# Optimization experiments

Hardware: AMD Instinct MI355X
Metric: run time of the kernel (lower is better)

The kernel has to match this reference:

```python
import jax, jax.numpy as jnp
import numpy as np

N_NODES = 20000
N_EDGES = 320000
N_RELS = 200
DESC_LEN = 16
DIM_G = 64
DIM_WORD = 300
DIM_HIDDEN = 256
H_DIR = DIM_HIDDEN // 2  # per-direction GRU hidden
N_CLASS = 2000
V_WORD = 30000
V_DESC = 30000
B, T = 4, 32


def setup_inputs() -> dict:
    key = jax.random.key(0)
    ks = jax.random.split(key, 24)
    inp = {}
    # index tensors (pad token is 0; generate tokens in [1, V) so all positions valid)
    inp['questions'] = jax.random.randint(ks[0], (B, T), 1, V_WORD)
    inp['node_descs'] = jax.random.randint(ks[1], (N_NODES, DESC_LEN), 1, V_DESC)
    inp['edge_src'] = jax.random.randint(ks[2], (N_EDGES,), 0, N_NODES)
    inp['edge_dst'] = jax.random.randint(ks[3], (N_EDGES,), 0, N_NODES)
    inp['edge_type'] = jax.random.randint(ks[4], (N_EDGES,), 0, N_RELS)
    # embeddings (normal with std 1/sqrt(dim) as in original init)
    inp['emb_word'] = jax.random.normal(ks[5], (V_WORD, DIM_WORD)) / np.sqrt(DIM_WORD)
    inp['emb_desc'] = jax.random.normal(ks[6], (V_DESC, DIM_G)) / np.sqrt(DIM_G)
    # BiGRU params (gates order r,z,n; concatenated along last dim)
    s = 0.1
    inp['Wx_f'] = jax.random.normal(ks[7], (DIM_WORD, 3 * H_DIR)) * s
    inp['Wh_f'] = jax.random.normal(ks[8], (H_DIR, 3 * H_DIR)) * s
    inp['bx_f'] = jnp.zeros((3 * H_DIR,))
    inp['bh_f'] = jnp.zeros((3 * H_DIR,))
    inp['Wx_b'] = jax.random.normal(ks[9], (DIM_WORD, 3 * H_DIR)) * s
    inp['Wh_b'] = jax.random.normal(ks[10], (H_DIR, 3 * H_DIR)) * s
    inp['bx_b'] = jnp.zeros((3 * H_DIR,))
    inp['bh_b'] = jnp.zeros((3 * H_DIR,))
    # lin_h_to_g (kaiming-ish scale)
    inp['W_hg'] = jax.random.normal(ks[11], (DIM_HIDDEN, DIM_G)) * np.sqrt(2.0 / DIM_HIDDEN)
    inp['b_hg'] = jnp.zeros((DIM_G,))
    # RGCN basis decomposition
    inp['bases'] = jax.random.normal(ks[12], (1, DIM_G, DIM_G)) * np.sqrt(1.0 / DIM_G)
    inp['w_comp'] = jax.random.normal(ks[13], (N_RELS, 1))
    inp['rgcn_bias'] = jnp.zeros((DIM_G,))
    # classifier
    inp['W1'] = jax.random.normal(ks[14], (DIM_G + DIM_HIDDEN, 1024)) * np.sqrt(2.0 / (DIM_G + DIM_HIDDEN))
    inp['b1'] = jnp.zeros((1024,))
    inp['W2'] = jax.random.normal(ks[15], (1024, N_CLASS)) * np.sqrt(2.0 / 1024)
    inp['b2'] = jnp.zeros((N_CLASS,))
    return inp


def _gru_last_hidden(x, mask, Wx, Wh, bx, bh):
    """Run a GRU over time; hidden only updates where mask is True.
    x: [B,T,D], mask: [B,T]. Returns final hidden [B,H]."""
    bsz = x.shape[0]
    h0 = jnp.zeros((bsz, Wh.shape[0]), x.dtype)
    gx_all = x @ Wx + bx  # [B,T,3H] precompute input gates

    def step(h, inputs):
        gx, mt = inputs  # [B,3H], [B]
        gh = h @ Wh + bh
        xr, xz, xn = jnp.split(gx, 3, axis=-1)
        hr, hz, hn = jnp.split(gh, 3, axis=-1)
        r = jax.nn.sigmoid(xr + hr)
        z = jax.nn.sigmoid(xz + hz)
        n = jnp.tanh(xn + r * hn)
        h_new = (1.0 - z) * n + z * h
        h = jnp.where(mt[:, None], h_new, h)
        return h, None

    hT, _ = jax.lax.scan(step, h0, (gx_all.transpose(1, 0, 2), mask.T))
    return hT


def _rel_graph_conv(h, edge_src, edge_dst, edge_type, bases, w_comp, bias):
    """Basis-decomposed RGCN layer (DGL RelGraphConv, norm=None, no self-loop).
    h: [B,N,G]. W_r = sum_k w_comp[r,k] * bases[k]."""
    n = h.shape[1]
    # project through each basis first: [B,N,K,O]
    hb = jnp.einsum('bng,kgo->bnko', h, bases)
    # per-edge message: gather src, combine with relation coefficients -> [B,E,O]
    msg = jnp.einsum('beko,ek->beo', hb[:, edge_src], w_comp[edge_type])
    # scatter-add to destination nodes
    agg = jax.vmap(lambda m: jax.ops.segment_sum(m, edge_dst, num_segments=n))(msg)
    return jax.nn.relu(agg + bias)


def reference(questions, node_descs, edge_src, edge_dst, edge_type,
              emb_word, emb_desc,
              Wx_f, Wh_f, bx_f, bh_f, Wx_b, Wh_b, bx_b, bh_b,
              W_hg, b_hg, bases, w_comp, rgcn_bias,
              W1, b1, W2, b2):
    # ---- question encoding (BiGRU over non-pad tokens; pad id = 0) ----
    mask = questions != 0  # [B,T]
    x = emb_word[questions]  # [B,T,Dw] (dropout is identity at eval)
    hf = _gru_last_hidden(x, mask, Wx_f, Wh_f, bx_f, bh_f)
    hb = _gru_last_hidden(x[:, ::-1], mask[:, ::-1], Wx_b, Wh_b, bx_b, bh_b)
    q_emb = jnp.concatenate([hf, hb], axis=-1)  # [B, dim_hidden]

    # ---- attention-weighted node features from descriptions ----
    desc_emb = emb_desc[node_descs]          # [N,L,G]
    q_g = q_emb @ W_hg + b_hg                # [B,G]
    attn1 = jax.nn.softmax(jnp.einsum('nlg,bg->bnl', desc_emb, q_g), axis=-1)
    node_feat = jnp.einsum('bnl,nlg->bng', attn1, desc_emb)  # [B,N,G]

    # ---- one RGCN hidden layer over the KB graph ----
    node_feat = _rel_graph_conv(node_feat, edge_src, edge_dst, edge_type,
                                bases, w_comp, rgcn_bias)

    # ---- attention pooling over nodes ----
    attn2 = jax.nn.softmax(jnp.einsum('bng,bg->bn', node_feat, q_g), axis=1)
    node_agg = jnp.einsum('bn,bng->bg', attn2, node_feat)    # [B,G]

    # ---- classifier ----
    feat = jnp.concatenate([node_agg, q_emb], axis=-1)       # [B, G+H]
    logits = jax.nn.relu(feat @ W1 + b1) @ W2 + b2           # [B, n_class]
    return logits
```

## Files before the change

kernel.cpp:

```cpp
#include <hip/hip_runtime.h>
#include <hip/hip_bf16.h>
#include <math.h>

typedef __hip_bfloat16 bf16;

#define NNODES 20000
#define NEDGES 320000
#define DLEN   16
#define G      64
#define DW     300
#define DH     256
#define HD     128
#define G3     384
#define NCLS   2000
#define NB     4
#define TT     32
#define VDESC  30000
#define NPART  5000
#define A2MID  64

#define NBLK_CVT   384
#define NBLK_GX2   1536
#define NBLK_DESCB (VDESC / 16)
#define NBLK_HIST  ((NEDGES + 255) / 256)
#define NBLK_W2T   (32 * 16)
#define NBLK_SCAT  ((NEDGES + 255) / 256)
#define NBLK_A1    (NNODES / 16)
#define NBLK_DQ    ((VDESC + 63) / 64)

__device__ __forceinline__ float ld(const float* p, size_t i) { return p[i]; }
__device__ __forceinline__ float ld(const bf16* p, size_t i) { return __bfloat162float(p[i]); }
__device__ __forceinline__ void st(float* p, size_t i, float v) { p[i] = v; }
__device__ __forceinline__ void st(bf16* p, size_t i, float v) { p[i] = __float2bfloat16(v); }
__device__ __forceinline__ float relu(float x) { return (x < 0.f) ? 0.f : x; }

#define OFF_FLAG  ((size_t)0)
#define OFF_GX    (OFF_FLAG + 4)
#define OFF_WHF   (OFF_GX   + 2*NB*TT*G3)
#define OFF_QEMB  (OFF_WHF  + 2*HD*G3)
#define OFF_QG    (OFF_QEMB + NB*DH)
#define OFF_HB    (OFF_QG   + NB*G)
#define OFF_DESCB (OFF_HB   + (size_t)NB*NNODES*G/2)
#define OFF_DQ    (OFF_DESCB + (size_t)VDESC*G/2)
#define OFF_PART  (OFF_DQ   + (size_t)VDESC*NB)
#define OFF_PART2 (OFF_PART + (size_t)NPART*NB*66)
#define OFF_DEG   (OFF_PART2+ (size_t)A2MID*NB*66)
#define OFF_OFFS  (OFF_DEG  + NNODES)
#define OFF_RANK  (OFF_OFFS + NNODES + 8)
#define OFF_EPACK (OFF_RANK + NEDGES)
#define OFF_HID   (OFF_EPACK + 2*(size_t)NEDGES)
#define OFF_W2T   (OFF_HID  + 4096)

__global__ void k_init(const unsigned* probe, int* flag, int* deg) {
    int i = blockIdx.x * 256 + threadIdx.x;
    if (i < NNODES) deg[i] = 0;
    if (blockIdx.x == 0 && threadIdx.x < 64) {
        int cnt = 0;
        for (int k = threadIdx.x; k < 4096; k += 64) {
            unsigned lo = probe[k] & 0xFFFFu;
            unsigned e = (lo >> 7) & 0xFFu;
            cnt += (e >= 0x66u && e <= 0x7Eu) ? 1 : 0;
        }
#pragma unroll
        for (int off = 1; off < 64; off <<= 1) cnt += __shfl_xor(cnt, off, 64);
        if (threadIdx.x == 0) *flag = (2 * cnt > 4096) ? 1 : 0;
    }
}

template <typename T>
__device__ void cvt_body(int id, const void* Whf_, const void* Whb_, float* whf) {
    if (id >= 2 * HD * G3) return;
    int d = id / (HD * G3), r = id % (HD * G3);
    const T* W = (const T*)(d ? Whb_ : Whf_);
    whf[id] = ld(W, (size_t)r);
}

template <typename T>
__device__ void gx2_body(int bx2, const int* questions, const void* emb_word_,
                         const void* Wxf_, const void* bxf_,
                         const void* Wxb_, const void* bxb_, float* gx,
                         float* xs, float* psum) {
    int tid = threadIdx.x;
    int jt = bx2 % 6;
    int rid = bx2 / 6;
    int step = rid & 31;
    int b = (rid >> 5) & 3;
    int d = rid >> 7;
    int t = d ? (TT - 1 - step) : step;
    int tok = questions[b * TT + t];
    const T* row = (const T*)emb_word_ + (size_t)tok * DW;
    for (int k = tid; k < DW; k += 256) xs[k] = ld(row, (size_t)k);
    __syncthreads();
    int lane = tid & 63, phase = tid >> 6;
    int j = jt * 64 + lane;
    const T* Wx = (const T*)(d ? Wxb_ : Wxf_);
    float acc = 0.f;
    int k0 = phase * 75;
#pragma unroll 15
    for (int kk = 0; kk < 75; kk++) {
        int k = k0 + kk;
        acc += xs[k] * ld(Wx, (size_t)k * G3 + j);
    }
    psum[tid] = acc;
    __syncthreads();
    if (phase == 0) {
        const T* bx = (const T*)(d ? bxb_ : bxf_);
        float tot = ld(bx, (size_t)j)
                  + psum[lane] + psum[64 + lane] + psum[128 + lane] + psum[192 + lane];
        gx[(size_t)rid * G3 + j] = tot;
    }
}

template <typename T>
__device__ void descb_body(int bx3, const void* emb_desc_, const void* bases_,
                           bf16* descB, float* bsm, float* rsm) {
    int tid = threadIdx.x;
    const T* bases = (const T*)bases_;
    const T* desc = (const T*)emb_desc_;
    for (int i = tid; i < G * G; i += 256) bsm[(i >> 6) * 68 + (i & 63)] = ld(bases, (size_t)i);
    int r0 = bx3 * 16;
    for (int i = tid; i < 16 * G; i += 256) {
        int r = i >> 6, k = i & 63;
        rsm[r * 68 + k] = ld(desc, (size_t)(r0 + r) * G + k);
    }
    __syncthreads();
    int g = tid & 63, slot = tid >> 6;
#pragma unroll
    for (int it = 0; it < 4; it++) {
        int r = slot * 4 + it;
        float acc = 0.f;
#pragma unroll 8
        for (int k = 0; k < G; k++) acc = fmaf(rsm[r * 68 + k], bsm[k * 68 + g], acc);
        descB[(size_t)(r0 + r) * G + g] = __float2bfloat16(acc);
    }
}

template <typename T>
__device__ void w2t_body(int bx5, const void* W2_, float* w2t, float* tile ) {
    int tid = threadIdx.x;
    int ct = bx5 >> 4, ut = bx5 & 15;
    int c0 = ct * 64, u0 = ut * 64;
    int lane = tid & 63, slot = tid >> 6;
    const T* W2 = (const T*)W2_;
    int c = c0 + lane;
    bool okc = (c < NCLS);
#pragma unroll
    for (int i = 0; i < 16; i++) {
        int u = slot * 16 + i;
        tile[u * 65 + lane] = okc ? ld(W2, (size_t)(u0 + u) * NCLS + c) : 0.f;
    }
    __syncthreads();
#pragma unroll
    for (int i = 0; i < 16; i++) {
        int cl = slot * 16 + i;
        if (c0 + cl < NCLS)
            w2t[(size_t)(c0 + cl) * 1024 + u0 + lane] = tile[lane * 65 + cl];
    }
}

__global__ void k_prep(const int* flag, const void* Whf, const void* Whb, float* whf,
                       const int* questions, const void* emb_word,
                       const void* Wxf, const void* bxf,
                       const void* Wxb, const void* bxb, float* gx,
                       const void* emb_desc, const void* bases, bf16* descB,
                       const int* edge_dst, int* deg, int* rank,
                       const void* W2, float* w2t) {
    __shared__ __align__(16) float smem[64 * 68 + 16 * 68];
    int bx = blockIdx.x;
    int tid = threadIdx.x;
    if (bx < NBLK_CVT) {
        int id = bx * 256 + tid;
        if (*flag) cvt_body<bf16>(id, Whf, Whb, whf);
        else       cvt_body<float>(id, Whf, Whb, whf);
    } else if (bx < NBLK_CVT + NBLK_GX2) {
        int bx2 = bx - NBLK_CVT;
        float* xs = smem;
        float* psum = smem + 320;
        if (*flag) gx2_body<bf16>(bx2, questions, emb_word, Wxf, bxf, Wxb, bxb, gx, xs, psum);
        else       gx2_body<float>(bx2, questions, emb_word, Wxf, bxf, Wxb, bxb, gx, xs, psum);
    } else if (bx < NBLK_CVT + NBLK_GX2 + NBLK_DESCB) {
        int bx3 = bx - NBLK_CVT - NBLK_GX2;
        float* bsm = smem;
        float* rsm = smem + 64 * 68;
        if (*flag) descb_body<bf16>(bx3, emb_desc, bases, descB, bsm, rsm);
        else       descb_body<float>(bx3, emb_desc, bases, descB, bsm, rsm);
    } else if (bx < NBLK_CVT + NBLK_GX2 + NBLK_DESCB + NBLK_HIST) {
        int e = (bx - NBLK_CVT - NBLK_GX2 - NBLK_DESCB) * 256 + tid;
        if (e < NEDGES) rank[e] = atomicAdd(&deg[edge_dst[e]], 1);
    } else {
        int bx5 = bx - NBLK_CVT - NBLK_GX2 - NBLK_DESCB - NBLK_HIST;
        if (*flag) w2t_body<bf16>(bx5, W2, w2t, smem);
        else       w2t_body<float>(bx5, W2, w2t, smem);
    }
}

template <typename T>
__device__ void gru_body(const int* questions, const float* gx, const float* whf,
                         const void* bhf_, const void* bhb_, float* qemb,
                         float* hsm, float* ghs) {
    int tid = threadIdx.x;
    int d = blockIdx.x >> 2, b = blockIdx.x & 3;
    int half = tid / G3, j = tid - half * G3;
    const float* wh = whf + (size_t)d * HD * G3 + (size_t)half * 64 * G3 + j;
    float w[64];
#pragma unroll
    for (int m = 0; m < 64; m++) w[m] = wh[(size_t)m * G3];
    const T* bh = (const T*)(d ? bhb_ : bhf_);
    float bhj = (half == 0) ? ld(bh, (size_t)j) : 0.f;
    if (tid < HD) hsm[tid] = 0.f;
    const float* gxb = gx + ((size_t)(d * NB + b)) * TT * G3;
    __syncthreads();
    const float4* h4 = (const float4*)(hsm + half * 64);
    for (int step = 0; step < TT; step++) {
        float acc = bhj;
#pragma unroll
        for (int m4 = 0; m4 < 16; m4++) {
            float4 hp = h4[m4];
            acc = fmaf(hp.x, w[4 * m4 + 0], acc);
            acc = fmaf(hp.y, w[4 * m4 + 1], acc);
            acc = fmaf(hp.z, w[4 * m4 + 2], acc);
            acc = fmaf(hp.w, w[4 * m4 + 3], acc);
        }
        ghs[half * G3 + j] = acc;
        __syncthreads();
        if (tid < HD) {
            const float* gxp = gxb + step * G3;
            int t = d ? (TT - 1 - step) : step;
            bool msk = questions[b * TT + t] != 0;
            float gr = ghs[tid] + ghs[G3 + tid];
            float gz = ghs[HD + tid] + ghs[G3 + HD + tid];
            float gn = ghs[2 * HD + tid] + ghs[G3 + 2 * HD + tid];
            float r = 1.f / (1.f + expf(-(gxp[tid] + gr)));
            float z = 1.f / (1.f + expf(-(gxp[HD + tid] + gz)));
            float n = tanhf(gxp[2 * HD + tid] + r * gn);
            float hn = (1.f - z) * n + z * hsm[tid];
            if (msk) hsm[tid] = hn;
        }
        __syncthreads();
    }
    if (tid < HD) qemb[b * DH + d * HD + tid] = hsm[tid];
}

__device__ void scan_body(const int* deg, int* offs, int* wtot) {
    int t = threadIdx.x;
    int lane = t & 63, wave = t >> 6;
    int c[27];
    int base = t * 27;
    int run = 0;
#pragma unroll
    for (int i = 0; i < 27; i++) {
        int v = (base + i < NNODES) ? deg[base + i] : 0;
        c[i] = run;
        run += v;
    }
    int myrun = run, inc = run;
#pragma unroll
    for (int off = 1; off < 64; off <<= 1) {
        int u = __shfl_up(inc, off, 64);
        if (lane >= off) inc += u;
    }
    if (lane == 63) wtot[wave] = inc;
    __syncthreads();
    if (t == 0) {
        int s = 0;
#pragma unroll
        for (int i = 0; i < 12; i++) { int v = wtot[i]; wtot[i] = s; s += v; }
        offs[NNODES] = s;
    }
    __syncthreads();
    int ebase = wtot[wave] + inc - myrun;
#pragma unroll
    for (int i = 0; i < 27; i++) {
        if (base + i < NNODES) offs[base + i] = ebase + c[i];
    }
}

__global__ __launch_bounds__(2 * G3) void k_gru(const int* flag, const int* questions,
                                                const float* gx, const float* whf,
                                                const void* bhf, const void* bhb, float* qemb,
                                                const int* deg, int* offs) {
    __shared__ __align__(16) float hsm[HD];
    __shared__ float ghs[2 * G3];
    __shared__ int wtot[12];
    if (blockIdx.x < 8) {
        if (*flag) gru_body<bf16>(questions, gx, whf, bhf, bhb, qemb, hsm, ghs);
        else       gru_body<float>(questions, gx, whf, bhf, bhb, qemb, hsm, ghs);
    } else {
        scan_body(deg, offs, wtot);
    }
}

template <typename T>
__device__ void qg_compute(const float* qemb, const void* W_hg_, const void* b_hg_,
                           float* out ) {
    int tid = threadIdx.x;
    int b = tid >> 6, g = tid & 63;
    const T* W = (const T*)W_hg_;
    float acc = ld((const T*)b_hg_, (size_t)g);
#pragma unroll 4
    for (int i = 0; i < DH; i++) acc += qemb[b * DH + i] * ld(W, (size_t)i * G + g);
    out[b * G + g] = acc;
}

template <typename T>
__device__ void dq_body(int chunk, const void* emb_desc_, const float* qgs, float* dq) {
    int tid = threadIdx.x;
    int ii = tid >> 2, b = tid & 3;
    int idx = chunk * 64 + ii;
    if (idx >= VDESC) return;
    const T* row = (const T*)emb_desc_ + (size_t)idx * G;
    const float* q = qgs + b * G;
    float acc = 0.f;
#pragma unroll 8
    for (int k = 0; k < G; k++) acc = fmaf(ld(row, (size_t)k), q[k], acc);
    dq[(size_t)idx * NB + b] = acc;
}

__global__ __launch_bounds__(256) void k_qg_dq(const int* flag, const float* qemb,
                                               const void* W_hg, const void* b_hg, float* qg,
                                               const void* emb_desc, float* dq) {
    __shared__ float qgs[NB * G];
    if (blockIdx.x == 0) {
        if (*flag) qg_compute<bf16>(qemb, W_hg, b_hg, qg);
        else       qg_compute<float>(qemb, W_hg, b_hg, qg);
        return;
    }
    if (*flag) qg_compute<bf16>(qemb, W_hg, b_hg, qgs);
    else       qg_compute<float>(qemb, W_hg, b_hg, qgs);
    __syncthreads();
    int chunk = blockIdx.x - 1;
    if (*flag) dq_body<bf16>(chunk, emb_desc, qgs, dq);
    else       dq_body<float>(chunk, emb_desc, qgs, dq);
}

template <typename T>
__device__ void scatter_body(int e, const int* src, const int* dst, const int* typ,
                             const void* w_comp_, const int* offs, const int* rank,
                             int2* epack) {
    if (e < NEDGES) {
        int pos = offs[dst[e]] + rank[e];
        int2 v;
        v.x = src[e];
        v.y = __float_as_int(ld((const T*)w_comp_, (size_t)typ[e]));
        epack[pos] = v;
    }
}

__device__ void attn1_body(int nb4, const int* node_descs, const float* dq,
                           const bf16* descB, bf16* hb16, float* attn_s, int* idxs) {
    int tid = threadIdx.x;
    int w = tid >> 6, lane = tid & 63;
    int n = nb4 * 4 + w;
    int b = lane >> 4, l = lane & 15;
    const int* nd = node_descs + n * DLEN;
    int idx = nd[l];
    float logit = dq[(size_t)idx * NB + b];
    float mx = logit;
#pragma unroll
    for (int off = 1; off < 16; off <<= 1) mx = fmaxf(mx, __shfl_xor(mx, off, 64));
    float e = expf(logit - mx);
    float s = e;
#pragma unroll
    for (int off = 1; off < 16; off <<= 1) s += __shfl_xor(s, off, 64);
    attn_s[w * 64 + lane] = e / s;
    if (lane < 16) idxs[w * 16 + lane] = idx;
    __syncthreads();
    float o0 = 0.f, o1 = 0.f, o2 = 0.f, o3 = 0.f;
#pragma unroll
    for (int ll = 0; ll < DLEN; ll++) {
        int row = idxs[w * 16 + ll];
        float v = __bfloat162float(descB[(size_t)row * G + lane]);
        o0 = fmaf(attn_s[w * 64 + ll], v, o0);
        o1 = fmaf(attn_s[w * 64 + 16 + ll], v, o1);
        o2 = fmaf(attn_s[w * 64 + 32 + ll], v, o2);
        o3 = fmaf(attn_s[w * 64 + 48 + ll], v, o3);
    }
    size_t baseo = (size_t)n * (NB * G) + lane;
    hb16[baseo + 0 * G] = __float2bfloat16(o0);
    hb16[baseo + 1 * G] = __float2bfloat16(o1);
    hb16[baseo + 2 * G] = __float2bfloat16(o2);
    hb16[baseo + 3 * G] = __float2bfloat16(o3);
}

__global__ __launch_bounds__(256) void k_sc_attn1(const int* flag,
                                                  const int* src, const int* dst, const int* typ,
                                                  const void* w_comp, const int* offs,
                                                  const int* rank, int2* epack,
                                                  const int* node_descs, const float* dq,
                                                  const bf16* descB, bf16* hb16) {
    __shared__ float attn_s[4 * 64];
    __shared__ int idxs[4 * DLEN];
    int bx = blockIdx.x;
    if (bx < NBLK_SCAT) {
        int e = bx * 256 + threadIdx.x;
        if (*flag) scatter_body<bf16>(e, src, dst, typ, w_comp, offs, rank, epack);
        else       scatter_body<float>(e, src, dst, typ, w_comp, offs, rank, epack);
    } else {
        int base = (bx - NBLK_SCAT) * 4;
        for (int it = 0; it < 4; it++) {
            if (it) __syncthreads();
            attn1_body(base + it, node_descs, dq, descB, hb16, attn_s, idxs);
        }
    }
}

__device__ __forceinline__ void a2_update(float& M, float& L, float& A, float p, float v) {
    if (p > M) {
        float s = expf(M - p);
        A *= s; L *= s; M = p;
    }
    float e = expf(p - M);
    L += e;
    A = fmaf(e, v, A);
}

template <typename T>
__device__ void agg_body(const bf16* hb16, const int* offs, const int2* epack,
                         const void* bias_, const float* qg, float* part) {
    int tid = threadIdx.x;
    int b = tid >> 6, g = tid & 63;
    int boff = b * G + g;
    float bias = ld((const T*)bias_, (size_t)g);
    float q = qg[b * G + g];
    float M = -3.4e38f, L = 0.f, A = 0.f;
#pragma unroll 1
    for (int it = 0; it < 4; it++) {
        int dn = blockIdx.x * 4 + it;
        int s0 = offs[dn], s1 = offs[dn + 1];
        float acc = 0.f;
        int p = s0;
        for (; p + 15 < s1; p += 16) {
            int2 ev[16]; float x[16];
#pragma unroll
            for (int k = 0; k < 16; k++) ev[k] = epack[p + k];
#pragma unroll
            for (int k = 0; k < 16; k++)
                x[k] = __bfloat162float(hb16[(size_t)ev[k].x * (NB * G) + boff]);
#pragma unroll
            for (int k = 0; k < 16; k++) acc += __int_as_float(ev[k].y) * x[k];
        }
        for (; p + 7 < s1; p += 8) {
            int2 ev[8]; float x[8];
#pragma unroll
            for (int k = 0; k < 8; k++) ev[k] = epack[p + k];
#pragma unroll
            for (int k = 0; k < 8; k++)
                x[k] = __bfloat162float(hb16[(size_t)ev[k].x * (NB * G) + boff]);
#pragma unroll
            for (int k = 0; k < 8; k++) acc += __int_as_float(ev[k].y) * x[k];
        }
        for (; p + 3 < s1; p += 4) {
            int2 ev[4]; float x[4];
#pragma unroll
            for (int k = 0; k < 4; k++) ev[k] = epack[p + k];
#pragma unroll
            for (int k = 0; k < 4; k++)
                x[k] = __bfloat162float(hb16[(size_t)ev[k].x * (NB * G) + boff]);
#pragma unroll
            for (int k = 0; k < 4; k++) acc += __int_as_float(ev[k].y) * x[k];
        }
        for (; p < s1; p++) {
            int2 ev = epack[p];
            acc += __int_as_float(ev.y) * __bfloat162float(hb16[(size_t)ev.x * (NB * G) + boff]);
        }
        float v = relu(acc + bias);
        float pl = v * q;
#pragma unroll
        for (int off = 32; off >= 1; off >>= 1) pl += __shfl_xor(pl, off, 64);
        a2_update(M, L, A, pl, v);
    }
    float* pp = part + ((size_t)blockIdx.x * NB + b) * 66;
    if (g == 0) { pp[0] = M; pp[1] = L; }
    pp[2 + g] = A;
}
__global__ __launch_bounds__(256) void k_agg(const int* flag, const bf16* hb16, const int* offs,
                                             const int2* epack, const void* bias,
                                             const float* qg, float* part) {
    if (*flag) agg_body<bf16>(hb16, offs, epack, bias, qg, part);
    else       agg_body<float>(hb16, offs, epack, bias, qg, part);
}

__global__ __launch_bounds__(256) void k_attn2m(const float* part, float* part2) {
    int tid = threadIdx.x;
    int b = tid >> 6, lane = tid & 63;
    int grp = blockIdx.x;
    const int per = (NPART + A2MID - 1) / A2MID;
    int start = grp * per;
    int end = (start + per < NPART) ? (start + per) : NPART;
    float M = -3.4e38f, L = 0.f, A = 0.f;
    for (int i = start; i < end; i++) {
        const float* pp = part + ((size_t)i * NB + b) * 66;
        float m = pp[0], l = pp[1], a = pp[2 + lane];
        float mn = fmaxf(M, m);
        float e1 = expf(M - mn), e2 = expf(m - mn);
        A = A * e1 + a * e2;
        L = L * e1 + l * e2;
        M = mn;
    }
    float* pq = part2 + ((size_t)grp * NB + b) * 66;
    if (lane == 0) { pq[0] = M; pq[1] = L; }
    pq[2 + lane] = A;
}

template <typename T>
__device__ void fc1_body(const float* part2, const float* qemb,
                         const void* W1_, const void* b1_, float* hid,
                         float* feat, float* psum) {
    int tid = threadIdx.x;
    int b = blockIdx.x >> 4, tile = blockIdx.x & 15;
    if (tid < 64) {
        float M = -3.4e38f, L = 0.f, A = 0.f;
        for (int p = 0; p < A2MID; p++) {
            const float* pp = part2 + ((size_t)p * NB + b) * 66;
            float m = pp[0], l = pp[1], a = pp[2 + tid];
            float mn = fmaxf(M, m);
            float e1 = expf(M - mn), e2 = expf(m - mn);
            A = A * e1 + a * e2;
            L = L * e1 + l * e2;
            M = mn;
        }
        feat[tid] = A / L;
        feat[tid + 256] = qemb[b * DH + tid + 192];
    } else {
        feat[tid] = qemb[b * DH + tid - G];
    }
    __syncthreads();
    int lane = tid & 63, phase = tid >> 6;
    int u = tile * 64 + lane;
    const T* W1 = (const T*)W1_;
    float acc = 0.f;
#pragma unroll 8
    for (int kk = 0; kk < 80; kk++) {
        int k = phase * 80 + kk;
        acc += feat[k] * ld(W1, (size_t)k * 1024 + u);
    }
    psum[tid] = acc;
    __syncthreads();
    if (phase == 0) {
        float tot = psum[lane] + psum[64 + lane] + psum[128 + lane] + psum[192 + lane]
                  + ld((const T*)b1_, (size_t)u);
        hid[b * 1024 + u] = relu(tot);
    }
}
__global__ __launch_bounds__(256) void k_fc1(const int* flag, const float* part2,
                                             const float* qemb, const void* W1, const void* b1,
                                             float* hid) {
    __shared__ float feat[320];
    __shared__ float psum[256];
    if (*flag) fc1_body<bf16>(part2, qemb, W1, b1, hid, feat, psum);
    else       fc1_body<float>(part2, qemb, W1, b1, hid, feat, psum);
}

template <typename T>
__device__ void fc2_body(const float* hid, const float* w2t, const void* b2_, void* out_,
                         float* hs) {
    int tid = threadIdx.x;
    for (int i = tid; i < 4096; i += 256) hs[i] = hid[i];
    __syncthreads();
    int lane = tid & 63, w = tid >> 6;
#pragma unroll
    for (int itc = 0; itc < 2; itc++) {
        int c = blockIdx.x * 8 + w * 2 + itc;
        const float* wrow = w2t + (size_t)c * 1024;
        float a0 = 0.f, a1 = 0.f, a2 = 0.f, a3 = 0.f;
#pragma unroll
        for (int i = 0; i < 16; i++) {
            int u = i * 64 + lane;
            float wv = wrow[u];
            a0 = fmaf(wv, hs[u], a0);
            a1 = fmaf(wv, hs[1024 + u], a1);
            a2 = fmaf(wv, hs[2048 + u], a2);
            a3 = fmaf(wv, hs[3072 + u], a3);
        }
#pragma unroll
        for (int off = 32; off >= 1; off >>= 1) {
            a0 += __shfl_xor(a0, off, 64);
            a1 += __shfl_xor(a1, off, 64);
            a2 += __shfl_xor(a2, off, 64);
            a3 += __shfl_xor(a3, off, 64);
        }
        if (lane < 4) {
            float av = (lane == 0) ? a0 : (lane == 1) ? a1 : (lane == 2) ? a2 : a3;
            st((T*)out_, (size_t)lane * NCLS + c, av + ld((const T*)b2_, (size_t)c));
        }
    }
}
__global__ __launch_bounds__(256) void k_fc2(const int* flag, const float* hid,
                                             const float* w2t, const void* b2v, void* out) {
    __shared__ float hs[4096];
    if (*flag) fc2_body<bf16>(hid, w2t, b2v, out, hs);
    else       fc2_body<float>(hid, w2t, b2v, out, hs);
}

extern "C" void kernel_launch(void* const* d_in, const int* in_sizes, int n_in,
                              void* d_out, int out_size, void* d_ws, size_t ws_size,
                              hipStream_t stream) {
    const int* questions  = (const int*)d_in[0];
    const int* node_descs = (const int*)d_in[1];
    const int* edge_src   = (const int*)d_in[2];
    const int* edge_dst   = (const int*)d_in[3];
    const int* edge_type  = (const int*)d_in[4];
    const void* emb_word  = d_in[5];
    const void* emb_desc  = d_in[6];
    const void* Wx_f = d_in[7];
    const void* Wh_f = d_in[8];
    const void* bx_f = d_in[9];
    const void* bh_f = d_in[10];
    const void* Wx_b = d_in[11];
    const void* Wh_b = d_in[12];
    const void* bx_b = d_in[13];
    const void* bh_b = d_in[14];
    const void* W_hg = d_in[15];
    const void* b_hg = d_in[16];
    const void* bases = d_in[17];
    const void* w_comp = d_in[18];
    const void* rgcn_bias = d_in[19];
    const void* W1 = d_in[20];
    const void* b1 = d_in[21];
    const void* W2 = d_in[22];
    const void* b2 = d_in[23];

    float* ws = (float*)d_ws;
    int*      flag  = (int*)(ws + OFF_FLAG);
    float*    gx    = ws + OFF_GX;
    float*    whf   = ws + OFF_WHF;
    float*    qemb  = ws + OFF_QEMB;
    float*    qg    = ws + OFF_QG;
    bf16*     hb16  = (bf16*)(ws + OFF_HB);
    bf16*     descB = (bf16*)(ws + OFF_DESCB);
    float*    dq    = ws + OFF_DQ;
    float*    part  = ws + OFF_PART;
    float*    part2 = ws + OFF_PART2;
    int*      deg   = (int*)(ws + OFF_DEG);
    int*      offs  = (int*)(ws + OFF_OFFS);
    int*      rank  = (int*)(ws + OFF_RANK);
    int2*     epack = (int2*)(ws + OFF_EPACK);
    float*    hid   = ws + OFF_HID;
    float*    w2t   = ws + OFF_W2T;

    hipLaunchKernelGGL(k_init, dim3(80), dim3(256), 0, stream,
                       (const unsigned*)emb_word, flag, deg);
    hipLaunchKernelGGL(k_prep,
                       dim3(NBLK_CVT + NBLK_GX2 + NBLK_DESCB + NBLK_HIST + NBLK_W2T),
                       dim3(256), 0, stream,
                       flag, Wh_f, Wh_b, whf,
                       questions, emb_word, Wx_f, bx_f, Wx_b, bx_b, gx,
                       emb_desc, bases, descB,
                       edge_dst, deg, rank, W2, w2t);
    hipLaunchKernelGGL(k_gru, dim3(9), dim3(2 * G3), 0, stream,
                       flag, questions, gx, whf, bh_f, bh_b, qemb, deg, offs);
    hipLaunchKernelGGL(k_qg_dq, dim3(1 + NBLK_DQ), dim3(256), 0, stream,
                       flag, qemb, W_hg, b_hg, qg, emb_desc, dq);
    hipLaunchKernelGGL(k_sc_attn1, dim3(NBLK_SCAT + NBLK_A1), dim3(256), 0, stream,
                       flag, edge_src, edge_dst, edge_type, w_comp, offs, rank, epack,
                       node_descs, dq, descB, hb16);
    hipLaunchKernelGGL(k_agg, dim3(NPART), dim3(256), 0, stream,
                       flag, hb16, offs, epack, rgcn_bias, qg, part);
    hipLaunchKernelGGL(k_attn2m, dim3(A2MID), dim3(256), 0, stream, part, part2);
    hipLaunchKernelGGL(k_fc1, dim3(NB * 16), dim3(256), 0, stream,
                       flag, part2, qemb, W1, b1, hid);
    hipLaunchKernelGGL(k_fc2, dim3(NCLS / 8), dim3(256), 0, stream,
                       flag, hid, w2t, b2, d_out);
}
```

Before: 326.6 us.

## Restructure RGCN aggregation to wave-per-node with LDS-staged edges and vector loads

The aggregation kernel now assigns one wavefront per destination node, with each lane handling 4 features of one batch via 8-byte vector loads of bf16 rows. The block's edge list is staged into shared memory before the gather. The per-block online softmax merge is done through shared memory after all four waves finish. Separately, the attention-1 blocks now process one node group per block instead of four, which quadruples that grid. The aim is fewer, wider gather loads and more parallelism, at the cost of extra syncs and shared-memory traffic.

```diff
diff --git a/kernel.cpp b/kernel.cpp
--- a/kernel.cpp
+++ b/kernel.cpp
@@ -18,6 +18,7 @@
 #define VDESC  30000
 #define NPART  5000
 #define A2MID  64
+#define MAXE   1024
 
 #define NBLK_CVT   384
 #define NBLK_GX2   1536
@@ -25,7 +26,7 @@
 #define NBLK_HIST  ((NEDGES + 255) / 256)
 #define NBLK_W2T   (32 * 16)
 #define NBLK_SCAT  ((NEDGES + 255) / 256)
-#define NBLK_A1    (NNODES / 16)
+#define NBLK_A1    (NNODES / 4)
 #define NBLK_DQ    ((VDESC + 63) / 64)
 
 __device__ __forceinline__ float ld(const float* p, size_t i) { return p[i]; }
@@ -33,6 +34,8 @@
 __device__ __forceinline__ void st(float* p, size_t i, float v) { p[i] = v; }
 __device__ __forceinline__ void st(bf16* p, size_t i, float v) { p[i] = __float2bfloat16(v); }
 __device__ __forceinline__ float relu(float x) { return (x < 0.f) ? 0.f : x; }
+__device__ __forceinline__ float bflo(unsigned u) { return __uint_as_float(u << 16); }
+__device__ __forceinline__ float bfhi(unsigned u) { return __uint_as_float(u & 0xffff0000u); }
 
 #define OFF_FLAG  ((size_t)0)
 #define OFF_GX    (OFF_FLAG + 4)
@@ -396,88 +399,95 @@
         if (*flag) scatter_body<bf16>(e, src, dst, typ, w_comp, offs, rank, epack);
         else       scatter_body<float>(e, src, dst, typ, w_comp, offs, rank, epack);
     } else {
-        int base = (bx - NBLK_SCAT) * 4;
-        for (int it = 0; it < 4; it++) {
-            if (it) __syncthreads();
-            attn1_body(base + it, node_descs, dq, descB, hb16, attn_s, idxs);
-        }
-    }
-}
-
-__device__ __forceinline__ void a2_update(float& M, float& L, float& A, float p, float v) {
-    if (p > M) {
-        float s = expf(M - p);
-        A *= s; L *= s; M = p;
-    }
-    float e = expf(p - M);
-    L += e;
-    A = fmaf(e, v, A);
+        attn1_body(bx - NBLK_SCAT, node_descs, dq, descB, hb16, attn_s, idxs);
+    }
 }
 
 template <typename T>
 __device__ void agg_body(const bf16* hb16, const int* offs, const int2* epack,
-                         const void* bias_, const float* qg, float* part) {
-    int tid = threadIdx.x;
-    int b = tid >> 6, g = tid & 63;
-    int boff = b * G + g;
-    float bias = ld((const T*)bias_, (size_t)g);
-    float q = qg[b * G + g];
+                         const void* bias_, const float* qg, float* part,
+                         int2* eL, float* pm ) {
+    int tid = threadIdx.x;
+    int w = tid >> 6, lane = tid & 63;
+    int b = lane >> 4, g0 = (lane & 15) << 2;
+    int nb = blockIdx.x * 4;
+    int e0 = offs[nb], e1 = offs[nb + 4];
+    int ne = e1 - e0;
+    int dn = nb + w;
+    int s0 = offs[dn] - e0, s1 = offs[dn + 1] - e0;
+    const char* hbase = (const char*)hb16 + (size_t)(b * G + g0) * 2;
+    float a0 = 0.f, a1 = 0.f, a2 = 0.f, a3 = 0.f;
+    for (int base = 0; base < ne; base += MAXE) {
+        int cnt = min(MAXE, ne - base);
+        __syncthreads();
+        for (int i = tid; i < cnt; i += 256) eL[i] = epack[(size_t)e0 + base + i];
+        __syncthreads();
+        int lo = max(s0 - base, 0), hi = min(s1 - base, cnt);
+        int p = lo;
+        for (; p + 7 < hi; p += 8) {
+            uint2 x[8]; float wv[8];
+#pragma unroll
+            for (int k = 0; k < 8; k++) {
+                int2 ev = eL[p + k];
+                wv[k] = __int_as_float(ev.y);
+                x[k] = *(const uint2*)(hbase + ((size_t)ev.x << 9));
+            }
+#pragma unroll
+            for (int k = 0; k < 8; k++) {
+                a0 = fmaf(wv[k], bflo(x[k].x), a0);
+                a1 = fmaf(wv[k], bfhi(x[k].x), a1);
+                a2 = fmaf(wv[k], bflo(x[k].y), a2);
+                a3 = fmaf(wv[k], bfhi(x[k].y), a3);
+            }
+        }
+        for (; p < hi; p++) {
+            int2 ev = eL[p];
+            float wvv = __int_as_float(ev.y);
+            uint2 x = *(const uint2*)(hbase + ((size_t)ev.x << 9));
+            a0 = fmaf(wvv, bflo(x.x), a0);
+            a1 = fmaf(wvv, bfhi(x.x), a1);
+            a2 = fmaf(wvv, bflo(x.y), a2);
+            a3 = fmaf(wvv, bfhi(x.y), a3);
+        }
+    }
+    float v0 = relu(a0 + ld((const T*)bias_, (size_t)(g0 + 0)));
+    float v1 = relu(a1 + ld((const T*)bias_, (size_t)(g0 + 1)));
+    float v2 = relu(a2 + ld((const T*)bias_, (size_t)(g0 + 2)));
+    float v3 = relu(a3 + ld((const T*)bias_, (size_t)(g0 + 3)));
+    const float* qb = qg + b * G + g0;
+    float pl = v0 * qb[0] + v1 * qb[1] + v2 * qb[2] + v3 * qb[3];
+#pragma unroll
+    for (int off = 1; off < 16; off <<= 1) pl += __shfl_xor(pl, off, 64);
+    float* pw = pm + (w * 4 + b) * 66;
+    pw[2 + g0 + 0] = v0;
+    pw[2 + g0 + 1] = v1;
+    pw[2 + g0 + 2] = v2;
+    pw[2 + g0 + 3] = v3;
+    if ((lane & 15) == 0) { pw[0] = pl; pw[1] = 1.f; }
+    __syncthreads();
+    int mb = tid >> 6, g = tid & 63;
     float M = -3.4e38f, L = 0.f, A = 0.f;
-#pragma unroll 1
-    for (int it = 0; it < 4; it++) {
-        int dn = blockIdx.x * 4 + it;
-        int s0 = offs[dn], s1 = offs[dn + 1];
-        float acc = 0.f;
-        int p = s0;
-        for (; p + 15 < s1; p += 16) {
-            int2 ev[16]; float x[16];
-#pragma unroll
-            for (int k = 0; k < 16; k++) ev[k] = epack[p + k];
-#pragma unroll
-            for (int k = 0; k < 16; k++)
-                x[k] = __bfloat162float(hb16[(size_t)ev[k].x * (NB * G) + boff]);
-#pragma unroll
-            for (int k = 0; k < 16; k++) acc += __int_as_float(ev[k].y) * x[k];
-        }
-        for (; p + 7 < s1; p += 8) {
-            int2 ev[8]; float x[8];
-#pragma unroll
-            for (int k = 0; k < 8; k++) ev[k] = epack[p + k];
-#pragma unroll
-            for (int k = 0; k < 8; k++)
-                x[k] = __bfloat162float(hb16[(size_t)ev[k].x * (NB * G) + boff]);
-#pragma unroll
-            for (int k = 0; k < 8; k++) acc += __int_as_float(ev[k].y) * x[k];
-        }
-        for (; p + 3 < s1; p += 4) {
-            int2 ev[4]; float x[4];
-#pragma unroll
-            for (int k = 0; k < 4; k++) ev[k] = epack[p + k];
-#pragma unroll
-            for (int k = 0; k < 4; k++)
-                x[k] = __bfloat162float(hb16[(size_t)ev[k].x * (NB * G) + boff]);
-#pragma unroll
-            for (int k = 0; k < 4; k++) acc += __int_as_float(ev[k].y) * x[k];
-        }
-        for (; p < s1; p++) {
-            int2 ev = epack[p];
-            acc += __int_as_float(ev.y) * __bfloat162float(hb16[(size_t)ev.x * (NB * G) + boff]);
-        }
-        float v = relu(acc + bias);
-        float pl = v * q;
-#pragma unroll
-        for (int off = 32; off >= 1; off >>= 1) pl += __shfl_xor(pl, off, 64);
-        a2_update(M, L, A, pl, v);
-    }
-    float* pp = part + ((size_t)blockIdx.x * NB + b) * 66;
+#pragma unroll
+    for (int i = 0; i < 4; i++) {
+        const float* ps = pm + (i * 4 + mb) * 66;
+        float m = ps[0], l = ps[1], a = ps[2 + g];
+        float mn = fmaxf(M, m);
+        float x1 = expf(M - mn), x2 = expf(m - mn);
+        A = A * x1 + a * x2;
+        L = L * x1 + l * x2;
+        M = mn;
+    }
+    float* pp = part + ((size_t)blockIdx.x * NB + mb) * 66;
     if (g == 0) { pp[0] = M; pp[1] = L; }
     pp[2 + g] = A;
 }
 __global__ __launch_bounds__(256) void k_agg(const int* flag, const bf16* hb16, const int* offs,
                                              const int2* epack, const void* bias,
                                              const float* qg, float* part) {
-    if (*flag) agg_body<bf16>(hb16, offs, epack, bias, qg, part);
-    else       agg_body<float>(hb16, offs, epack, bias, qg, part);
+    __shared__ int2 eL[MAXE];
+    __shared__ float pm[4 * 4 * 66];
+    if (*flag) agg_body<bf16>(hb16, offs, epack, bias, qg, part, eL, pm);
+    else       agg_body<float>(hb16, offs, epack, bias, qg, part, eL, pm);
 }
 
 __global__ __launch_bounds__(256) void k_attn2m(const float* part, float* part2) {
```

Result: faster. 308.2 us (-5.6%).
